# Optimization experiments

Hardware: AMD Instinct MI355X
Metric: run time of the kernel (lower is better)

Reference implementation:

```python
import jax, jax.numpy as jnp
import numpy as np

NB, DIM, DSTATE, DCONV, EXPAND = 4, 256, 16, 4, 2
DIN = EXPAND * DIM                 # 512
DTRANK = (DIM + 15) // 16          # 16, mamba-ssm default dt_rank = ceil(d_model/16)
B, L = 16, 512


def layer_norm(x, w, b, eps=1e-5):
    mu = x.mean(-1, keepdims=True)
    var = x.var(-1, keepdims=True)
    return (x - mu) * jax.lax.rsqrt(var + eps) * w + b


def selective_scan(u, delta, A, Bm, Cm, D):
    # u, delta: (B,L,DIN); Bm,Cm: (B,L,N); A: (DIN,N); D: (DIN,)
    def step(h, xs):
        d_t, B_t, C_t, u_t = xs          # (B,DIN), (B,N), (B,N), (B,DIN)
        dA = jnp.exp(d_t[..., None] * A)                                  # (B,DIN,N)
        h = dA * h + d_t[..., None] * B_t[:, None, :] * u_t[..., None]   # (B,DIN,N)
        y = jnp.einsum('bdn,bn->bd', h, C_t)
        return h, y

    h0 = jnp.zeros((u.shape[0], u.shape[2], A.shape[1]), u.dtype)
    xs = (delta.transpose(1, 0, 2), Bm.transpose(1, 0, 2),
          Cm.transpose(1, 0, 2), u.transpose(1, 0, 2))
    _, ys = jax.lax.scan(step, h0, xs)
    return ys.transpose(1, 0, 2) + u * D


def mamba_block(x, ln_w, ln_b, in_w, in_b, cw, cb, xp_w, dtw, dtb, A_log, D, ow):
    h = layer_norm(x, ln_w, ln_b)
    xz = h @ in_w.T + in_b                       # (B,L,2*DIN)
    xin, z = xz[..., :DIN], xz[..., DIN:]
    # causal depthwise conv over the sequence dim
    xc = jax.lax.conv_general_dilated(
        xin.transpose(0, 2, 1), cw[:, None, :], (1,), [(DCONV - 1, 0)],
        dimension_numbers=('NCH', 'OIH', 'NCH'), feature_group_count=DIN)
    xc = jax.nn.silu(xc + cb[None, :, None]).transpose(0, 2, 1)   # (B,L,DIN)
    dbc = xc @ xp_w.T                                             # (B,L,DTRANK+2*N)
    dt = jax.nn.softplus(dbc[..., :DTRANK] @ dtw.T + dtb)         # (B,L,DIN)
    Bm = dbc[..., DTRANK:DTRANK + DSTATE]
    Cm = dbc[..., DTRANK + DSTATE:]
    y = selective_scan(xc, dt, -jnp.exp(A_log), Bm, Cm, D)
    return x + (y * jax.nn.silu(z)) @ ow.T       # dropout = identity at eval


def setup_inputs() -> dict:
    key = jax.random.key(0)
    ks = jax.random.split(key, 8)
    s = 0.02
    A_log = jnp.tile(jnp.log(jnp.arange(1, DSTATE + 1, dtype=jnp.float32))[None, None, :],
                     (NB, DIN, 1))
    return {
        'x': jax.random.normal(ks[0], (B, L, DIM), jnp.float32),
        'ln_w': jnp.ones((NB, DIM), jnp.float32),
        'ln_b': jnp.zeros((NB, DIM), jnp.float32),
        'in_proj_w': jax.random.normal(ks[1], (NB, 2 * DIN, DIM), jnp.float32) * s,
        'in_proj_b': jnp.zeros((NB, 2 * DIN), jnp.float32),
        'conv_w': jax.random.normal(ks[2], (NB, DIN, DCONV), jnp.float32) * s,
        'conv_b': jnp.zeros((NB, DIN), jnp.float32),
        'x_proj_w': jax.random.normal(ks[3], (NB, DTRANK + 2 * DSTATE, DIN), jnp.float32) * s,
        'dt_proj_w': jax.random.normal(ks[4], (NB, DIN, DTRANK), jnp.float32) * s,
        'dt_proj_b': jax.random.uniform(ks[5], (NB, DIN), jnp.float32, -4.0, -3.0),
        'A_log': A_log,
        'D': jnp.ones((NB, DIN), jnp.float32),
        'out_proj_w': jax.random.normal(ks[6], (NB, DIM, DIN), jnp.float32) * s,
    }


def reference(x, ln_w, ln_b, in_proj_w, in_proj_b, conv_w, conv_b, x_proj_w,
              dt_proj_w, dt_proj_b, A_log, D, out_proj_w):
    for i in range(NB):
        x = mamba_block(x, ln_w[i], ln_b[i], in_proj_w[i], in_proj_b[i],
                        conv_w[i], conv_b[i], x_proj_w[i], dt_proj_w[i],
                        dt_proj_b[i], A_log[i], D[i], out_proj_w[i])
    return x
```

## Files before the change

kernel.cpp:

```cpp
#include <hip/hip_runtime.h>
#include <math.h>

#define NB 4
#define DIMM 256
#define DSTATE 16
#define DCONV 4
#define DIN 512
#define DTRANK 16
#define BB 16
#define LL 512
#define TT (BB * LL)
#define XZ_DIM (2 * DIN)
#define DBC_DIM (DTRANK + 2 * DSTATE)
#define NC 32
#define CHUNK (LL / NC)

__device__ __forceinline__ unsigned short f2bf(float f) {
    union { float f; unsigned int u; } v; v.f = f;
    unsigned int r = v.u + 0x7fff + ((v.u >> 16) & 1);
    return (unsigned short)(r >> 16);
}
__device__ __forceinline__ float bf2f(unsigned short u) {
    union { unsigned int i; float f; } v; v.i = ((unsigned int)u) << 16;
    return v.f;
}

__global__ __launch_bounds__(256) void cvt3_kernel(const float* __restrict__ s1,
                                                   unsigned short* __restrict__ d1, int n1,
                                                   const float* __restrict__ s2,
                                                   unsigned short* __restrict__ d2, int n2,
                                                   const float* __restrict__ s3,
                                                   unsigned short* __restrict__ d3, int n3) {
    int stride = gridDim.x * 256;
    for (int i = blockIdx.x * 256 + threadIdx.x; i < n1; i += stride) {
        float4 v = ((const float4*)s1)[i];
        ushort4 o; o.x = f2bf(v.x); o.y = f2bf(v.y); o.z = f2bf(v.z); o.w = f2bf(v.w);
        ((ushort4*)d1)[i] = o;
    }
    for (int i = blockIdx.x * 256 + threadIdx.x; i < n2; i += stride) {
        float4 v = ((const float4*)s2)[i];
        ushort4 o; o.x = f2bf(v.x); o.y = f2bf(v.y); o.z = f2bf(v.z); o.w = f2bf(v.w);
        ((ushort4*)d2)[i] = o;
    }
    for (int i = blockIdx.x * 256 + threadIdx.x; i < n3; i += stride) {
        float4 v = ((const float4*)s3)[i];
        ushort4 o; o.x = f2bf(v.x); o.y = f2bf(v.y); o.z = f2bf(v.z); o.w = f2bf(v.w);
        ((ushort4*)d3)[i] = o;
    }
}

__global__ __launch_bounds__(256) void ln_kernel(const float* __restrict__ x,
                                                 const float* __restrict__ w,
                                                 const float* __restrict__ bvec,
                                                 unsigned short* __restrict__ out) {
    int t = blockIdx.x;
    int i = threadIdx.x;
    float v = x[t * DIMM + i];
    float s = v, s2 = v * v;
#pragma unroll
    for (int off = 1; off < 64; off <<= 1) {
        s  += __shfl_xor(s, off);
        s2 += __shfl_xor(s2, off);
    }
    __shared__ float ss[4], ss2[4];
    int wid = i >> 6;
    if ((i & 63) == 0) { ss[wid] = s; ss2[wid] = s2; }
    __syncthreads();
    s  = ss[0] + ss[1] + ss[2] + ss[3];
    s2 = ss2[0] + ss2[1] + ss2[2] + ss2[3];
    float mu  = s * (1.0f / DIMM);
    float var = s2 * (1.0f / DIMM) - mu * mu;
    float r   = rsqrtf(var + 1e-5f);
    out[t * DIMM + i] = f2bf((v - mu) * r * w[i] + bvec[i]);
}

#define TBM 128
#define TBN 64
#define TBK 32
#define LDKW (TBK + 8)
__global__ __launch_bounds__(256) void gemm_bf16(const unsigned short* __restrict__ A, int lda,
                                                 const unsigned short* __restrict__ Bw, int ldb,
                                                 const float* __restrict__ bias,
                                                 const float* __restrict__ resid,
                                                 float* __restrict__ C,
                                                 unsigned short* __restrict__ C1b,
                                                 unsigned short* __restrict__ C2b, int nsplit,
                                                 int ldc, int N, int K) {
    using short8  = __attribute__((ext_vector_type(8))) short;
    using floatx4 = __attribute__((ext_vector_type(4))) float;
    __shared__ __align__(16) unsigned short As[TBM * LDKW];
    __shared__ __align__(16) unsigned short Bs[TBN * LDKW];

    int tid  = threadIdx.x;
    int m0   = blockIdx.y * TBM;
    int n0   = blockIdx.x * TBN;
    int w    = tid >> 6;
    int lane = tid & 63;
    int wm   = (w & 1) * 64;
    int wn   = (w >> 1) * 32;
    int lr   = lane & 15;
    int quad = lane >> 4;

    floatx4 acc[4][2] = {};

    int ar = tid >> 1;
    int ak = (tid & 1) * 16;
    int br = tid >> 2;
    int bk = (tid & 3) * 8;

    for (int k0 = 0; k0 < K; k0 += TBK) {
        {
            const unsigned short* src = &A[(size_t)(m0 + ar) * lda + k0 + ak];
            int4 a0 = *(const int4*)(src);
            int4 a1 = *(const int4*)(src + 8);
            *(int4*)&As[ar * LDKW + ak]     = a0;
            *(int4*)&As[ar * LDKW + ak + 8] = a1;
        }
        {
            int gn = n0 + br;
            int4 b0 = make_int4(0, 0, 0, 0);
            if (gn < N) b0 = *(const int4*)&Bw[(size_t)gn * ldb + k0 + bk];
            *(int4*)&Bs[br * LDKW + bk] = b0;
        }
        __syncthreads();
        short8 af[4], bf[2];
#pragma unroll
        for (int i = 0; i < 4; ++i)
            af[i] = *(const short8*)&As[(wm + i * 16 + lr) * LDKW + quad * 8];
#pragma unroll
        for (int j = 0; j < 2; ++j)
            bf[j] = *(const short8*)&Bs[(wn + j * 16 + lr) * LDKW + quad * 8];
#pragma unroll
        for (int i = 0; i < 4; ++i)
#pragma unroll
            for (int j = 0; j < 2; ++j)
                acc[i][j] = __builtin_amdgcn_mfma_f32_16x16x32_bf16(af[i], bf[j], acc[i][j], 0, 0, 0);
        __syncthreads();
    }

#pragma unroll
    for (int j = 0; j < 2; ++j) {
        int cn = n0 + wn + j * 16 + lr;
        if (cn < N) {
            float bb = bias ? bias[cn] : 0.0f;
            if (C1b) {
                unsigned short* dst = (cn < nsplit) ? C1b : C2b;
                int col = (cn < nsplit) ? cn : cn - nsplit;
#pragma unroll
                for (int i = 0; i < 4; ++i)
#pragma unroll
                    for (int r = 0; r < 4; ++r) {
                        int cm = m0 + wm + i * 16 + quad * 4 + r;
                        dst[(size_t)cm * ldc + col] = f2bf(acc[i][j][r] + bb);
                    }
            } else {
#pragma unroll
                for (int i = 0; i < 4; ++i)
#pragma unroll
                    for (int r = 0; r < 4; ++r) {
                        int cm = m0 + wm + i * 16 + quad * 4 + r;
                        float v = acc[i][j][r] + bb;
                        if (resid) v += resid[(size_t)cm * ldc + cn];
                        C[(size_t)cm * ldc + cn] = v;
                    }
            }
        }
    }
}

__global__ __launch_bounds__(256) void conv_silu(const unsigned short* __restrict__ Xb,
                                                 const float* __restrict__ cw,
                                                 const float* __restrict__ cb,
                                                 unsigned short* __restrict__ xcb) {
    int idx = blockIdx.x * blockDim.x + threadIdx.x;
    int d = idx & (DIN - 1);
    int t = idx >> 9;
    int l = t & (LL - 1);
    int bq = t >> 9;
    float acc = cb[d];
#pragma unroll
    for (int k = 0; k < DCONV; ++k) {
        int ls = l - (DCONV - 1) + k;
        if (ls >= 0) acc += cw[d * DCONV + k] * bf2f(Xb[(size_t)(bq * LL + ls) * DIN + d]);
    }
    float v = acc / (1.0f + __expf(-acc));
    xcb[(size_t)t * DIN + d] = f2bf(v);
}

__global__ __launch_bounds__(256) void dt_kernel(const float* __restrict__ dbc,
                                                 const float* __restrict__ dtw,
                                                 const float* __restrict__ dtbias,
                                                 unsigned short* __restrict__ dtout) {
    int idx = blockIdx.x * blockDim.x + threadIdx.x;
    int d = idx & (DIN - 1);
    int t = idx >> 9;
    float a = dtbias[d];
    const float4* wv = (const float4*)(dtw + d * DTRANK);
    const float* dr = dbc + (size_t)t * DBC_DIM;
#pragma unroll
    for (int q = 0; q < 4; ++q) {
        float4 w4 = wv[q];
        a += w4.x * dr[q * 4 + 0] + w4.y * dr[q * 4 + 1] +
             w4.z * dr[q * 4 + 2] + w4.w * dr[q * 4 + 3];
    }
    float sp = (a > 20.0f) ? a : log1pf(__expf(a));
    dtout[(size_t)t * DIN + d] = f2bf(sp);
}

__global__ __launch_bounds__(256) void scan_p1(const unsigned short* __restrict__ xcb,
                                               const unsigned short* __restrict__ dtb,
                                               const float* __restrict__ dbc,
                                               const float* __restrict__ A_log,
                                               float* __restrict__ S,
                                               float* __restrict__ H) {
    int bid = blockIdx.x;
    int dq = bid & 3;
    int c  = (bid >> 2) & (NC - 1);
    int b  = bid >> 7;
    int dloc = threadIdx.x >> 1;
    int sh   = threadIdx.x & 1;
    int d  = dq * 128 + dloc;
    int n0 = sh * 8;
    int base = b * LL + c * CHUNK;

    __shared__ float LB[CHUNK * DBC_DIM];
    for (int i = threadIdx.x; i < CHUNK * DBC_DIM / 4; i += 256)
        ((float4*)LB)[i] = ((const float4*)(dbc + (size_t)base * DBC_DIM))[i];

    float a[8];
    {
        const float4* ar = (const float4*)(A_log + d * DSTATE + n0);
        float4 v0 = ar[0], v1 = ar[1];
        a[0] = -__expf(v0.x); a[1] = -__expf(v0.y); a[2] = -__expf(v0.z); a[3] = -__expf(v0.w);
        a[4] = -__expf(v1.x); a[5] = -__expf(v1.y); a[6] = -__expf(v1.z); a[7] = -__expf(v1.w);
    }
    __syncthreads();

    float h[8];
#pragma unroll
    for (int j = 0; j < 8; ++j) h[j] = 0.0f;
    float Ssum = 0.0f;
    float u   = bf2f(xcb[(size_t)base * DIN + d]);
    float dtv = bf2f(dtb[(size_t)base * DIN + d]);
#pragma unroll 4
    for (int s = 0; s < CHUNK; ++s) {
        float nu  = bf2f(xcb[(size_t)(base + s + 1) * DIN + d]);
        float ndt = bf2f(dtb[(size_t)(base + s + 1) * DIN + d]);
        const float* row = &LB[s * DBC_DIM];
        Ssum += dtv;
        float wv = dtv * u;
#pragma unroll
        for (int j = 0; j < 8; ++j) {
            float dA = __expf(dtv * a[j]);
            h[j] = dA * h[j] + wv * row[DTRANK + n0 + j];
        }
        u = nu; dtv = ndt;
    }
    size_t sc = (size_t)b * NC + c;
    if (sh == 0) S[sc * DIN + d] = Ssum;
#pragma unroll
    for (int j = 0; j < 8; ++j) H[(sc * DIN + d) * 16 + n0 + j] = h[j];
}

__global__ __launch_bounds__(256) void scan_p2(const float* __restrict__ A_log,
                                               const float* __restrict__ S,
                                               float* __restrict__ H) {
    int idx = blockIdx.x * 256 + threadIdx.x;
    int n = idx & 15;
    int d = (idx >> 4) & (DIN - 1);
    int b = idx >> 13;
    float a = -__expf(A_log[d * DSTATE + n]);
    float h = 0.0f;
#pragma unroll
    for (int c = 0; c < NC; ++c) {
        size_t sc = (size_t)b * NC + c;
        float Sv = S[sc * DIN + d];
        size_t q = (sc * DIN + d) * 16 + n;
        float Hc = H[q];
        H[q] = h;
        h = __expf(a * Sv) * h + Hc;
    }
}

__global__ __launch_bounds__(256) void scan_p3(const unsigned short* __restrict__ xcb,
                                               const unsigned short* __restrict__ dtb,
                                               const unsigned short* __restrict__ Zb,
                                               const float* __restrict__ dbc,
                                               const float* __restrict__ A_log,
                                               const float* __restrict__ Dp,
                                               const float* __restrict__ Hin,
                                               unsigned short* __restrict__ gb) {
    int bid = blockIdx.x;
    int dq = bid & 3;
    int c  = (bid >> 2) & (NC - 1);
    int b  = bid >> 7;
    int dloc = threadIdx.x >> 1;
    int sh   = threadIdx.x & 1;
    int d  = dq * 128 + dloc;
    int n0 = sh * 8;
    int base = b * LL + c * CHUNK;

    __shared__ float LB[CHUNK * DBC_DIM];
    for (int i = threadIdx.x; i < CHUNK * DBC_DIM / 4; i += 256)
        ((float4*)LB)[i] = ((const float4*)(dbc + (size_t)base * DBC_DIM))[i];

    float a[8];
    {
        const float4* ar = (const float4*)(A_log + d * DSTATE + n0);
        float4 v0 = ar[0], v1 = ar[1];
        a[0] = -__expf(v0.x); a[1] = -__expf(v0.y); a[2] = -__expf(v0.z); a[3] = -__expf(v0.w);
        a[4] = -__expf(v1.x); a[5] = -__expf(v1.y); a[6] = -__expf(v1.z); a[7] = -__expf(v1.w);
    }
    float Dd = Dp[d];
    size_t sc = (size_t)b * NC + c;
    float h[8];
#pragma unroll
    for (int j = 0; j < 8; ++j) h[j] = Hin[(sc * DIN + d) * 16 + n0 + j];
    __syncthreads();

    float u   = bf2f(xcb[(size_t)base * DIN + d]);
    float dtv = bf2f(dtb[(size_t)base * DIN + d]);
#pragma unroll 4
    for (int s = 0; s < CHUNK; ++s) {
        float nu  = bf2f(xcb[(size_t)(base + s + 1) * DIN + d]);
        float ndt = bf2f(dtb[(size_t)(base + s + 1) * DIN + d]);
        const float* row = &LB[s * DBC_DIM];
        float wv = dtv * u;
        float y  = (sh == 0) ? u * Dd : 0.0f;
#pragma unroll
        for (int j = 0; j < 8; ++j) {
            float dA = __expf(dtv * a[j]);
            h[j] = dA * h[j] + wv * row[DTRANK + n0 + j];
            y += h[j] * row[DTRANK + DSTATE + n0 + j];
        }
        y += __shfl_xor(y, 1);
        if (sh == 0) {
            float zf = bf2f(Zb[(size_t)(base + s) * DIN + d]);
            float g = y * (zf / (1.0f + __expf(-zf)));
            gb[(size_t)(base + s) * DIN + d] = f2bf(g);
        }
        u = nu; dtv = ndt;
    }
}

extern "C" void kernel_launch(void* const* d_in, const int* in_sizes, int n_in,
                              void* d_out, int out_size, void* d_ws, size_t ws_size,
                              hipStream_t stream) {
    const float* x_in   = (const float*)d_in[0];
    const float* ln_w   = (const float*)d_in[1];
    const float* ln_b   = (const float*)d_in[2];
    const float* in_w   = (const float*)d_in[3];
    const float* in_b   = (const float*)d_in[4];
    const float* conv_w = (const float*)d_in[5];
    const float* conv_b = (const float*)d_in[6];
    const float* xp_w   = (const float*)d_in[7];
    const float* dt_w   = (const float*)d_in[8];
    const float* dt_b   = (const float*)d_in[9];
    const float* A_log  = (const float*)d_in[10];
    const float* Dp     = (const float*)d_in[11];
    const float* ow     = (const float*)d_in[12];
    float* out = (float*)d_out;

    const size_t M = 1048576;
    float* ws = (float*)d_ws;
    float* xbuf = ws;
    unsigned short* hb  = (unsigned short*)(ws + 2 * M);
    float* dbc = ws + 3 * M;
    unsigned short* Xb  = (unsigned short*)(ws + 4 * M);
    unsigned short* Zb  = (unsigned short*)(ws + 6 * M);
    unsigned short* xcb = (unsigned short*)(ws + 8 * M);
    unsigned short* dtb = (unsigned short*)(ws + 10 * M);
    unsigned short* gb  = (unsigned short*)(ws + 12 * M);
    float* Hbuf = ws + 14 * M;
    float* Sbuf = ws + 18 * M;
    unsigned short* inwb = (unsigned short*)(ws + 18 * M + 262144);
    unsigned short* owb  = inwb + (size_t)NB * XZ_DIM * DIMM;
    unsigned short* xpwb = owb + (size_t)NB * DIMM * DIN;

    cvt3_kernel<<<256, 256, 0, stream>>>(
        in_w, inwb, NB * XZ_DIM * DIMM / 4,
        ow,   owb,  NB * DIMM * DIN / 4,
        xp_w, xpwb, NB * DBC_DIM * DIN / 4);

    for (int layer = 0; layer < NB; ++layer) {
        const float* xi = (layer == 0) ? x_in : xbuf;
        float* xo = (layer == NB - 1) ? out : xbuf;

        ln_kernel<<<TT, 256, 0, stream>>>(xi, ln_w + layer * DIMM, ln_b + layer * DIMM, hb);

        gemm_bf16<<<dim3(XZ_DIM / TBN, TT / TBM), 256, 0, stream>>>(
            hb, DIMM, inwb + (size_t)layer * XZ_DIM * DIMM, DIMM,
            in_b + layer * XZ_DIM, nullptr, nullptr, Xb, Zb, DIN, DIN, XZ_DIM, DIMM);

        conv_silu<<<(TT * DIN) / 256, 256, 0, stream>>>(
            Xb, conv_w + layer * DIN * DCONV, conv_b + layer * DIN, xcb);

        gemm_bf16<<<dim3(1, TT / TBM), 256, 0, stream>>>(
            xcb, DIN, xpwb + (size_t)layer * DBC_DIM * DIN, DIN,
            nullptr, nullptr, dbc, nullptr, nullptr, 0, DBC_DIM, DBC_DIM, DIN);

        dt_kernel<<<(TT * DIN) / 256, 256, 0, stream>>>(
            dbc, dt_w + (size_t)layer * DIN * DTRANK, dt_b + layer * DIN, dtb);

        const float* Al = A_log + (size_t)layer * DIN * DSTATE;
        scan_p1<<<BB * NC * 4, 256, 0, stream>>>(xcb, dtb, dbc, Al, Sbuf, Hbuf);
        scan_p2<<<(BB * DIN * 16) / 256, 256, 0, stream>>>(Al, Sbuf, Hbuf);
        scan_p3<<<BB * NC * 4, 256, 0, stream>>>(xcb, dtb, Zb, dbc, Al,
                                                 Dp + layer * DIN, Hbuf, gb);

        gemm_bf16<<<dim3(DIMM / TBN, TT / TBM), 256, 0, stream>>>(
            gb, DIN, owb + (size_t)layer * DIMM * DIN, DIN,
            nullptr, xi, xo, nullptr, nullptr, 0, DIMM, DIMM, DIN);
    }
}
```

Baseline: 688.9 us.

## Add 128x128 MFMA GEMM with direct global-to-LDS loads for in/out projections

Adds a new bf16 MFMA GEMM for the in_proj and out_proj matmuls. It uses 128x128 tiles with a 4x4 MFMA block per wave and loads A/B tiles straight into LDS with global_load_lds, skipping the register staging step. The old kernel is kept as a slimmed-down gemm_small for the narrow x_proj matmul, with no bias, residual or split-store branches. Larger tiles raise data reuse per block, but they cut the block count for out_proj to 128, and the unpadded LDS layout may cause bank conflicts.

```diff
diff --git a/kernel.cpp b/kernel.cpp
--- a/kernel.cpp
+++ b/kernel.cpp
@@ -25,6 +25,12 @@
     return v.f;
 }
 
+__device__ __forceinline__ void gl_lds16(const unsigned short* g, unsigned short* l) {
+    __builtin_amdgcn_global_load_lds(
+        (const __attribute__((address_space(1))) unsigned int*)g,
+        (__attribute__((address_space(3))) unsigned int*)l, 16, 0, 0);
+}
+
 __global__ __launch_bounds__(256) void cvt3_kernel(const float* __restrict__ s1,
                                                    unsigned short* __restrict__ d1, int n1,
                                                    const float* __restrict__ s2,
@@ -74,18 +80,99 @@
     out[t * DIMM + i] = f2bf((v - mu) * r * w[i] + bvec[i]);
 }
 
-#define TBM 128
-#define TBN 64
-#define TBK 32
-#define LDKW (TBK + 8)
-__global__ __launch_bounds__(256) void gemm_bf16(const unsigned short* __restrict__ A, int lda,
+#define GTM 128
+#define GTN 128
+#define GTK 32
+__global__ __launch_bounds__(256) void gemm_mfma(const unsigned short* __restrict__ A, int lda,
                                                  const unsigned short* __restrict__ Bw, int ldb,
                                                  const float* __restrict__ bias,
                                                  const float* __restrict__ resid,
                                                  float* __restrict__ C,
                                                  unsigned short* __restrict__ C1b,
                                                  unsigned short* __restrict__ C2b, int nsplit,
-                                                 int ldc, int N, int K) {
+                                                 int ldc, int K) {
+    using short8  = __attribute__((ext_vector_type(8))) short;
+    using floatx4 = __attribute__((ext_vector_type(4))) float;
+    __shared__ __align__(16) unsigned short As[GTM * GTK];
+    __shared__ __align__(16) unsigned short Bs[GTN * GTK];
+
+    int tid  = threadIdx.x;
+    int m0   = blockIdx.y * GTM;
+    int n0   = blockIdx.x * GTN;
+    int w    = tid >> 6;
+    int lane = tid & 63;
+    int wm   = (w & 1) * 64;
+    int wn   = (w >> 1) * 64;
+    int lr   = lane & 15;
+    int quad = lane >> 4;
+
+    int srow = lane >> 2;
+    int scol = (lane & 3) * 8;
+
+    floatx4 acc[4][4] = {};
+
+    for (int k0 = 0; k0 < K; k0 += GTK) {
+#pragma unroll
+        for (int t = 0; t < 2; ++t) {
+            const unsigned short* ga =
+                &A[(size_t)(m0 + w * 32 + t * 16 + srow) * lda + k0 + scol];
+            gl_lds16(ga, &As[w * 1024 + t * 512]);
+            const unsigned short* gb =
+                &Bw[(size_t)(n0 + w * 32 + t * 16 + srow) * ldb + k0 + scol];
+            gl_lds16(gb, &Bs[w * 1024 + t * 512]);
+        }
+        __syncthreads();
+        short8 af[4], bf[4];
+#pragma unroll
+        for (int i = 0; i < 4; ++i)
+            af[i] = *(const short8*)&As[(wm + i * 16 + lr) * GTK + quad * 8];
+#pragma unroll
+        for (int j = 0; j < 4; ++j)
+            bf[j] = *(const short8*)&Bs[(wn + j * 16 + lr) * GTK + quad * 8];
+#pragma unroll
+        for (int i = 0; i < 4; ++i)
+#pragma unroll
+            for (int j = 0; j < 4; ++j)
+                acc[i][j] = __builtin_amdgcn_mfma_f32_16x16x32_bf16(af[i], bf[j], acc[i][j], 0, 0, 0);
+        __syncthreads();
+    }
+
+#pragma unroll
+    for (int j = 0; j < 4; ++j) {
+        int cn = n0 + wn + j * 16 + lr;
+        float bb = bias ? bias[cn] : 0.0f;
+        if (C1b) {
+            unsigned short* dst = (cn < nsplit) ? C1b : C2b;
+            int col = (cn < nsplit) ? cn : cn - nsplit;
+#pragma unroll
+            for (int i = 0; i < 4; ++i)
+#pragma unroll
+                for (int r = 0; r < 4; ++r) {
+                    int cm = m0 + wm + i * 16 + quad * 4 + r;
+                    dst[(size_t)cm * ldc + col] = f2bf(acc[i][j][r] + bb);
+                }
+        } else {
+#pragma unroll
+            for (int i = 0; i < 4; ++i)
+#pragma unroll
+                for (int r = 0; r < 4; ++r) {
+                    int cm = m0 + wm + i * 16 + quad * 4 + r;
+                    float v = acc[i][j][r] + bb;
+                    if (resid) v += resid[(size_t)cm * ldc + cn];
+                    C[(size_t)cm * ldc + cn] = v;
+                }
+        }
+    }
+}
+
+#define TBM 128
+#define TBN 64
+#define TBK 32
+#define LDKW (TBK + 8)
+__global__ __launch_bounds__(256) void gemm_small(const unsigned short* __restrict__ A, int lda,
+                                                  const unsigned short* __restrict__ Bw, int ldb,
+                                                  float* __restrict__ C, int ldc,
+                                                  int N, int K) {
     using short8  = __attribute__((ext_vector_type(8))) short;
     using floatx4 = __attribute__((ext_vector_type(4))) float;
     __shared__ __align__(16) unsigned short As[TBM * LDKW];
@@ -142,28 +229,13 @@
     for (int j = 0; j < 2; ++j) {
         int cn = n0 + wn + j * 16 + lr;
         if (cn < N) {
-            float bb = bias ? bias[cn] : 0.0f;
-            if (C1b) {
-                unsigned short* dst = (cn < nsplit) ? C1b : C2b;
-                int col = (cn < nsplit) ? cn : cn - nsplit;
-#pragma unroll
-                for (int i = 0; i < 4; ++i)
-#pragma unroll
-                    for (int r = 0; r < 4; ++r) {
-                        int cm = m0 + wm + i * 16 + quad * 4 + r;
-                        dst[(size_t)cm * ldc + col] = f2bf(acc[i][j][r] + bb);
-                    }
-            } else {
-#pragma unroll
-                for (int i = 0; i < 4; ++i)
-#pragma unroll
-                    for (int r = 0; r < 4; ++r) {
-                        int cm = m0 + wm + i * 16 + quad * 4 + r;
-                        float v = acc[i][j][r] + bb;
-                        if (resid) v += resid[(size_t)cm * ldc + cn];
-                        C[(size_t)cm * ldc + cn] = v;
-                    }
-            }
+#pragma unroll
+            for (int i = 0; i < 4; ++i)
+#pragma unroll
+                for (int r = 0; r < 4; ++r) {
+                    int cm = m0 + wm + i * 16 + quad * 4 + r;
+                    C[(size_t)cm * ldc + cn] = acc[i][j][r];
+                }
         }
     }
 }
@@ -388,16 +460,16 @@
 
         ln_kernel<<<TT, 256, 0, stream>>>(xi, ln_w + layer * DIMM, ln_b + layer * DIMM, hb);
 
-        gemm_bf16<<<dim3(XZ_DIM / TBN, TT / TBM), 256, 0, stream>>>(
+        gemm_mfma<<<dim3(XZ_DIM / GTN, TT / GTM), 256, 0, stream>>>(
             hb, DIMM, inwb + (size_t)layer * XZ_DIM * DIMM, DIMM,
-            in_b + layer * XZ_DIM, nullptr, nullptr, Xb, Zb, DIN, DIN, XZ_DIM, DIMM);
+            in_b + layer * XZ_DIM, nullptr, nullptr, Xb, Zb, DIN, DIN, DIMM);
 
         conv_silu<<<(TT * DIN) / 256, 256, 0, stream>>>(
             Xb, conv_w + layer * DIN * DCONV, conv_b + layer * DIN, xcb);
 
-        gemm_bf16<<<dim3(1, TT / TBM), 256, 0, stream>>>(
+        gemm_small<<<dim3(1, TT / TBM), 256, 0, stream>>>(
             xcb, DIN, xpwb + (size_t)layer * DBC_DIM * DIN, DIN,
-            nullptr, nullptr, dbc, nullptr, nullptr, 0, DBC_DIM, DBC_DIM, DIN);
+            dbc, DBC_DIM, DBC_DIM, DIN);
 
         dt_kernel<<<(TT * DIN) / 256, 256, 0, stream>>>(
             dbc, dt_w + (size_t)layer * DIN * DTRANK, dt_b + layer * DIN, dtb);
@@ -408,8 +480,8 @@
         scan_p3<<<BB * NC * 4, 256, 0, stream>>>(xcb, dtb, Zb, dbc, Al,
                                                  Dp + layer * DIN, Hbuf, gb);
 
-        gemm_bf16<<<dim3(DIMM / TBN, TT / TBM), 256, 0, stream>>>(
+        gemm_mfma<<<dim3(DIMM / GTN, TT / GTM), 256, 0, stream>>>(
             gb, DIN, owb + (size_t)layer * DIMM * DIN, DIN,
-            nullptr, xi, xo, nullptr, nullptr, 0, DIMM, DIMM, DIN);
-    }
-}
+            nullptr, xi, xo, nullptr, nullptr, 0, DIMM, DIN);
+    }
+}
```

Result: slower. 709.4 us (+3.0%).

## Fuse three-pass chunked scan into single decoupled-lookback kernel

Applied to the files above, without the earlier changes.

Replaces the three scan kernels (chunk-local pass, sequential carry pass, output pass) with one kernel. Blocks take chunk indices from an atomic ticket and publish their chunk aggregates and inclusive prefixes with flags. Each block then looks back over earlier chunks to build its carry before running the output pass, which removes two launches and the separate carry kernel. The chunk count is halved to 16, which lengthens each block's serial work, and the design depends on spin-waiting plus per-call flag zeroing.

```diff
diff --git a/kernel.cpp b/kernel.cpp
--- a/kernel.cpp
+++ b/kernel.cpp
@@ -12,8 +12,9 @@
 #define TT (BB * LL)
 #define XZ_DIM (2 * DIN)
 #define DBC_DIM (DTRANK + 2 * DSTATE)
-#define NC 32
-#define CHUNK (LL / NC)
+#define NCC 16
+#define CHK (LL / NCC)
+#define ESTR 4224
 
 __device__ __forceinline__ unsigned short f2bf(float f) {
     union { float f; unsigned int u; } v; v.f = f;
@@ -23,6 +24,17 @@
 __device__ __forceinline__ float bf2f(unsigned short u) {
     union { unsigned int i; float f; } v; v.i = ((unsigned int)u) << 16;
     return v.f;
+}
+__device__ __forceinline__ float agload(const float* p) {
+    return __hip_atomic_load(p, __ATOMIC_RELAXED, __HIP_MEMORY_SCOPE_AGENT);
+}
+__device__ __forceinline__ void agstore(float* p, float v) {
+    __hip_atomic_store(p, v, __ATOMIC_RELAXED, __HIP_MEMORY_SCOPE_AGENT);
+}
+
+__global__ __launch_bounds__(256) void zero_kernel(int* __restrict__ p, int n) {
+    int i = blockIdx.x * 256 + threadIdx.x;
+    if (i < n) p[i] = 0;
 }
 
 __global__ __launch_bounds__(256) void cvt3_kernel(const float* __restrict__ s1,
@@ -207,24 +219,32 @@
     dtout[(size_t)t * DIN + d] = f2bf(sp);
 }
 
-__global__ __launch_bounds__(256) void scan_p1(const unsigned short* __restrict__ xcb,
-                                               const unsigned short* __restrict__ dtb,
-                                               const float* __restrict__ dbc,
-                                               const float* __restrict__ A_log,
-                                               float* __restrict__ S,
-                                               float* __restrict__ H) {
-    int bid = blockIdx.x;
-    int dq = bid & 3;
-    int c  = (bid >> 2) & (NC - 1);
-    int b  = bid >> 7;
+__global__ __launch_bounds__(256) void scan_fused(const unsigned short* __restrict__ xcb,
+                                                  const unsigned short* __restrict__ dtb,
+                                                  const unsigned short* __restrict__ Zb,
+                                                  const float* __restrict__ dbc,
+                                                  const float* __restrict__ A_log,
+                                                  const float* __restrict__ Dp,
+                                                  float* __restrict__ pub,
+                                                  int* __restrict__ flags,
+                                                  int* __restrict__ ticket,
+                                                  unsigned short* __restrict__ gb) {
+    __shared__ float LB[CHK * DBC_DIM];
+    __shared__ int tkt_s;
+    if (threadIdx.x == 0) tkt_s = atomicAdd(ticket, 1);
+    __syncthreads();
+    int t = tkt_s;
+    int c = t >> 6;
+    int chain = t & 63;
+    int b  = chain >> 2;
+    int dq = chain & 3;
     int dloc = threadIdx.x >> 1;
     int sh   = threadIdx.x & 1;
     int d  = dq * 128 + dloc;
     int n0 = sh * 8;
-    int base = b * LL + c * CHUNK;
-
-    __shared__ float LB[CHUNK * DBC_DIM];
-    for (int i = threadIdx.x; i < CHUNK * DBC_DIM / 4; i += 256)
+    int base = b * LL + c * CHK;
+
+    for (int i = threadIdx.x; i < CHK * DBC_DIM / 4; i += 256)
         ((float4*)LB)[i] = ((const float4*)(dbc + (size_t)base * DBC_DIM))[i];
 
     float a[8];
@@ -243,7 +263,7 @@
     float u   = bf2f(xcb[(size_t)base * DIN + d]);
     float dtv = bf2f(dtb[(size_t)base * DIN + d]);
 #pragma unroll 4
-    for (int s = 0; s < CHUNK; ++s) {
+    for (int s = 0; s < CHK; ++s) {
         float nu  = bf2f(xcb[(size_t)(base + s + 1) * DIN + d]);
         float ndt = bf2f(dtb[(size_t)(base + s + 1) * DIN + d]);
         const float* row = &LB[s * DBC_DIM];
@@ -256,72 +276,73 @@
         }
         u = nu; dtv = ndt;
     }
-    size_t sc = (size_t)b * NC + c;
-    if (sh == 0) S[sc * DIN + d] = Ssum;
-#pragma unroll
-    for (int j = 0; j < 8; ++j) H[(sc * DIN + d) * 16 + n0 + j] = h[j];
-}
-
-__global__ __launch_bounds__(256) void scan_p2(const float* __restrict__ A_log,
-                                               const float* __restrict__ S,
-                                               float* __restrict__ H) {
-    int idx = blockIdx.x * 256 + threadIdx.x;
-    int n = idx & 15;
-    int d = (idx >> 4) & (DIN - 1);
-    int b = idx >> 13;
-    float a = -__expf(A_log[d * DSTATE + n]);
-    float h = 0.0f;
-#pragma unroll
-    for (int c = 0; c < NC; ++c) {
-        size_t sc = (size_t)b * NC + c;
-        float Sv = S[sc * DIN + d];
-        size_t q = (sc * DIN + d) * 16 + n;
-        float Hc = H[q];
-        H[q] = h;
-        h = __expf(a * Sv) * h + Hc;
-    }
-}
-
-__global__ __launch_bounds__(256) void scan_p3(const unsigned short* __restrict__ xcb,
-                                               const unsigned short* __restrict__ dtb,
-                                               const unsigned short* __restrict__ Zb,
-                                               const float* __restrict__ dbc,
-                                               const float* __restrict__ A_log,
-                                               const float* __restrict__ Dp,
-                                               const float* __restrict__ Hin,
-                                               unsigned short* __restrict__ gb) {
-    int bid = blockIdx.x;
-    int dq = bid & 3;
-    int c  = (bid >> 2) & (NC - 1);
-    int b  = bid >> 7;
-    int dloc = threadIdx.x >> 1;
-    int sh   = threadIdx.x & 1;
-    int d  = dq * 128 + dloc;
-    int n0 = sh * 8;
-    int base = b * LL + c * CHUNK;
-
-    __shared__ float LB[CHUNK * DBC_DIM];
-    for (int i = threadIdx.x; i < CHUNK * DBC_DIM / 4; i += 256)
-        ((float4*)LB)[i] = ((const float4*)(dbc + (size_t)base * DBC_DIM))[i];
-
-    float a[8];
-    {
-        const float4* ar = (const float4*)(A_log + d * DSTATE + n0);
-        float4 v0 = ar[0], v1 = ar[1];
-        a[0] = -__expf(v0.x); a[1] = -__expf(v0.y); a[2] = -__expf(v0.z); a[3] = -__expf(v0.w);
-        a[4] = -__expf(v1.x); a[5] = -__expf(v1.y); a[6] = -__expf(v1.z); a[7] = -__expf(v1.w);
-    }
+
+    float* ent = pub + (size_t)t * ESTR;
+    int last = (c == NCC - 1);
+
+    if (!last && c > 0) {
+        if (sh == 0) agstore(&ent[dloc], Ssum);
+#pragma unroll
+        for (int j = 0; j < 8; ++j) agstore(&ent[128 + dloc * 16 + n0 + j], h[j]);
+        __threadfence();
+        __syncthreads();
+        if (threadIdx.x == 0)
+            __hip_atomic_store(&flags[t], 1, __ATOMIC_RELEASE, __HIP_MEMORY_SCOPE_AGENT);
+    }
+
+    float carry[8];
+    if (c == 0) {
+#pragma unroll
+        for (int j = 0; j < 8; ++j) carry[j] = 0.0f;
+    } else {
+        float accp[8], acch[8];
+#pragma unroll
+        for (int j = 0; j < 8; ++j) { accp[j] = 1.0f; acch[j] = 0.0f; }
+        int cp = c - 1;
+        while (true) {
+            int fidx = (cp << 6) | chain;
+            int fv;
+            do {
+                fv = __hip_atomic_load(&flags[fidx], __ATOMIC_ACQUIRE, __HIP_MEMORY_SCOPE_AGENT);
+                if (fv == 0) __builtin_amdgcn_s_sleep(2);
+            } while (fv == 0);
+            const float* e = pub + (size_t)fidx * ESTR;
+            if (fv == 2) {
+#pragma unroll
+                for (int j = 0; j < 8; ++j)
+                    carry[j] = acch[j] + accp[j] * agload(&e[2176 + dloc * 16 + n0 + j]);
+                break;
+            } else {
+                float Sc = agload(&e[dloc]);
+#pragma unroll
+                for (int j = 0; j < 8; ++j) {
+                    acch[j] += accp[j] * agload(&e[128 + dloc * 16 + n0 + j]);
+                    accp[j] *= __expf(a[j] * Sc);
+                }
+                --cp;
+            }
+        }
+    }
+
+    if (!last) {
+#pragma unroll
+        for (int j = 0; j < 8; ++j) {
+            float hi = carry[j] * __expf(a[j] * Ssum) + h[j];
+            agstore(&ent[2176 + dloc * 16 + n0 + j], hi);
+        }
+        __threadfence();
+        __syncthreads();
+        if (threadIdx.x == 0)
+            __hip_atomic_store(&flags[t], 2, __ATOMIC_RELEASE, __HIP_MEMORY_SCOPE_AGENT);
+    }
+
     float Dd = Dp[d];
-    size_t sc = (size_t)b * NC + c;
-    float h[8];
-#pragma unroll
-    for (int j = 0; j < 8; ++j) h[j] = Hin[(sc * DIN + d) * 16 + n0 + j];
-    __syncthreads();
-
-    float u   = bf2f(xcb[(size_t)base * DIN + d]);
-    float dtv = bf2f(dtb[(size_t)base * DIN + d]);
+#pragma unroll
+    for (int j = 0; j < 8; ++j) h[j] = carry[j];
+    u   = bf2f(xcb[(size_t)base * DIN + d]);
+    dtv = bf2f(dtb[(size_t)base * DIN + d]);
 #pragma unroll 4
-    for (int s = 0; s < CHUNK; ++s) {
+    for (int s = 0; s < CHK; ++s) {
         float nu  = bf2f(xcb[(size_t)(base + s + 1) * DIN + d]);
         float ndt = bf2f(dtb[(size_t)(base + s + 1) * DIN + d]);
         const float* row = &LB[s * DBC_DIM];
@@ -371,11 +392,13 @@
     unsigned short* xcb = (unsigned short*)(ws + 8 * M);
     unsigned short* dtb = (unsigned short*)(ws + 10 * M);
     unsigned short* gb  = (unsigned short*)(ws + 12 * M);
-    float* Hbuf = ws + 14 * M;
-    float* Sbuf = ws + 18 * M;
-    unsigned short* inwb = (unsigned short*)(ws + 18 * M + 262144);
+    float* pub = ws + 14 * M;
+    int* flagsBase = (int*)(ws + 18 * M + 262144);
+    unsigned short* inwb = (unsigned short*)(ws + 18 * M + 524288);
     unsigned short* owb  = inwb + (size_t)NB * XZ_DIM * DIMM;
     unsigned short* xpwb = owb + (size_t)NB * DIMM * DIN;
+
+    zero_kernel<<<(4 * 1024 + 4 + 255) / 256, 256, 0, stream>>>(flagsBase, 4 * 1024 + 4);
 
     cvt3_kernel<<<256, 256, 0, stream>>>(
         in_w, inwb, NB * XZ_DIM * DIMM / 4,
@@ -402,11 +425,10 @@
         dt_kernel<<<(TT * DIN) / 256, 256, 0, stream>>>(
             dbc, dt_w + (size_t)layer * DIN * DTRANK, dt_b + layer * DIN, dtb);
 
-        const float* Al = A_log + (size_t)layer * DIN * DSTATE;
-        scan_p1<<<BB * NC * 4, 256, 0, stream>>>(xcb, dtb, dbc, Al, Sbuf, Hbuf);
-        scan_p2<<<(BB * DIN * 16) / 256, 256, 0, stream>>>(Al, Sbuf, Hbuf);
-        scan_p3<<<BB * NC * 4, 256, 0, stream>>>(xcb, dtb, Zb, dbc, Al,
-                                                 Dp + layer * DIN, Hbuf, gb);
+        scan_fused<<<BB * NCC * 4, 256, 0, stream>>>(
+            xcb, dtb, Zb, dbc, A_log + (size_t)layer * DIN * DSTATE,
+            Dp + layer * DIN, pub, flagsBase + layer * 1024,
+            flagsBase + 4096 + layer, gb);
 
         gemm_bf16<<<dim3(DIMM / TBN, TT / TBM), 256, 0, stream>>>(
             gb, DIN, owb + (size_t)layer * DIMM * DIN, DIN,
```

Result: slower. 2.220 ms (+222.3%).
